# Performance work log

Hardware: AMD Instinct MI355X
Metric: run time of the kernel (lower is better)

Reference implementation:

```python
import jax, jax.numpy as jnp
import numpy as np

B, T, D, H, HORIZON, OUT = 1024, 64, 128, 128, 24, 1
ATT = 64  # attention MLP hidden size


def _p(key, shape, scale=0.05):
    return scale * jax.random.normal(key, shape, dtype=jnp.float32)


def setup_inputs() -> dict:
    ks = jax.random.split(jax.random.key(0), 20)
    return dict(
        X=jax.random.normal(ks[0], (B, T, D), jnp.float32),
        y_hist=jax.random.normal(ks[1], (B, T), jnp.float32),
        We_w=_p(ks[2], (ATT, 2 * H + 1)), We_b=_p(ks[3], (ATT,)),
        ve_w=_p(ks[4], (1, ATT)), ve_b=_p(ks[5], (1,)),
        enc_Wih=_p(ks[6], (4 * H, D)), enc_Whh=_p(ks[7], (4 * H, H)),
        enc_bih=_p(ks[8], (4 * H,)), enc_bhh=_p(ks[9], (4 * H,)),
        dec_Wih=_p(ks[10], (4 * H, 1)), dec_Whh=_p(ks[11], (4 * H, H)),
        dec_bih=_p(ks[12], (4 * H,)), dec_bhh=_p(ks[13], (4 * H,)),
        Wd_w=_p(ks[14], (ATT, 3 * H)), Wd_b=_p(ks[15], (ATT,)),
        vd_w=_p(ks[16], (1, ATT)), vd_b=_p(ks[17], (1,)),
        fc_w=_p(ks[18], (OUT, 2 * H + T)), fc_b=_p(ks[19], (OUT,)),
    )


def _lstm_cell(x, h, c, Wih, Whh, bih, bhh):
    # torch.nn.LSTMCell gate order: i, f, g, o
    gates = x @ Wih.T + bih + h @ Whh.T + bhh
    i, f, g, o = jnp.split(gates, 4, axis=1)
    c2 = jax.nn.sigmoid(f) * c + jax.nn.sigmoid(i) * jnp.tanh(g)
    h2 = jax.nn.sigmoid(o) * jnp.tanh(c2)
    return h2, c2


def _forward(X, y_hist, We_w, We_b, ve_w, ve_b,
             enc_Wih, enc_Whh, enc_bih, enc_bhh,
             dec_Wih, dec_Whh, dec_bih, dec_bhh,
             Wd_w, Wd_b, vd_w, vd_b, fc_w, fc_b):
    batch = X.shape[0]
    # --- encoder with input attention (vectorized over the per-k python loop) ---
    W_hs = We_w[:, :2 * H]       # weights on [h_prev, s_prev]
    w_feat = We_w[:, 2 * H]      # weight on the scalar feature, shape (ATT,)

    def enc_step(carry, x_t):
        h, c = carry
        base = jnp.concatenate([h, c], axis=1) @ W_hs.T + We_b        # (B, ATT)
        energy = jnp.tanh(base[:, None, :] + x_t[:, :, None] * w_feat)  # (B, D, ATT)
        scores = energy @ ve_w[0] + ve_b[0]                            # (B, D)
        alpha = jax.nn.softmax(scores, axis=1)
        x_tilde = alpha * x_t
        h2, c2 = _lstm_cell(x_tilde, h, c, enc_Wih, enc_Whh, enc_bih, enc_bhh)
        return (h2, c2), h2

    h0 = jnp.zeros((batch, H), X.dtype)
    c0 = jnp.zeros((batch, H), X.dtype)
    _, enc_h = jax.lax.scan(enc_step, (h0, c0), X.transpose(1, 0, 2))
    enc_hiddens = enc_h.transpose(1, 0, 2)  # (B, T, H)

    # --- decoder with temporal attention ---
    # Wd_w columns ordered as cat([encoder_hiddens, d_prev, c_prev])
    enc_proj = jnp.einsum('bth,kh->btk', enc_hiddens, Wd_w[:, :H])  # (B, T, ATT)
    Wd_d, Wd_c = Wd_w[:, H:2 * H], Wd_w[:, 2 * H:]

    def dec_step(carry, _):
        d, cc, y_prev = carry
        dc = d @ Wd_d.T + cc @ Wd_c.T + Wd_b                # (B, ATT)
        energy = jnp.tanh(enc_proj + dc[:, None, :])         # (B, T, ATT)
        score = energy @ vd_w[0] + vd_b[0]                   # (B, T)
        beta = jax.nn.softmax(score, axis=1)
        context = jnp.einsum('bt,bth->bh', beta, enc_hiddens)  # (B, H)
        d2, cc2 = _lstm_cell(y_prev, d, cc, dec_Wih, dec_Whh, dec_bih, dec_bhh)
        fc_in = jnp.concatenate([d2, context, y_hist], axis=1)  # (B, 2H+T)
        out = fc_in @ fc_w.T + fc_b                              # (B, 1)
        return (d2, cc2, out), out

    d0 = jnp.zeros((batch, H), X.dtype)
    cd0 = jnp.zeros((batch, H), X.dtype)
    y0 = y_hist[:, -1:]
    _, outs = jax.lax.scan(dec_step, (d0, cd0, y0), None, length=HORIZON)
    return outs.transpose(1, 0, 2)  # (B, horizon, output_dim)


def reference(X, y_hist, We_w, We_b, ve_w, ve_b,
              enc_Wih, enc_Whh, enc_bih, enc_bhh,
              dec_Wih, dec_Whh, dec_bih, dec_bhh,
              Wd_w, Wd_b, vd_w, vd_b, fc_w, fc_b):
    return _forward(X, y_hist, We_w, We_b, ve_w, ve_b,
                    enc_Wih, enc_Whh, enc_bih, enc_bhh,
                    dec_Wih, dec_Whh, dec_bih, dec_bhh,
                    Wd_w, Wd_b, vd_w, vd_b, fc_w, fc_b)
```

## Files before the change

### kernel.cpp

```cpp
#include <hip/hip_runtime.h>
#include <hip/hip_bf16.h>


#define B_    1024
#define T_    64
#define D_    128
#define H_    128
#define HOR_  24
#define ATT_  64
#define BB    4
#define LOG2E 1.4426950408889634f
#define C127  (1.f/127.f)
#define KLAG  8.245856315e-05f

typedef float f32x4  __attribute__((ext_vector_type(4)));
typedef short bf16x8 __attribute__((ext_vector_type(8)));
typedef int   i32x4  __attribute__((ext_vector_type(4)));

#define MFMA16(a,b,c) __builtin_amdgcn_mfma_f32_16x16x32_bf16((a),(b),(c),0,0,0)
#define MFMAI8(a,b,c) __builtin_amdgcn_mfma_i32_16x16x64_i8((a),(b),(c),0,0,0)

#define WHS_E    0
#define WDDC_E   16384
#define WDENC_E  32768
#define WENC8_B  81920
#define WDEC8_B  212992
#define SENC_B   278528
#define SDEC_B   280576

__device__ __forceinline__ short f2b(float f) {
  union { float f; unsigned u; } c; c.f = f;
  unsigned r = c.u + 0x7fffu + ((c.u >> 16) & 1u);
  return (short)(r >> 16);
}
__device__ __forceinline__ float b2f(short s) {
  union { unsigned u; float f; } c; c.u = ((unsigned)(unsigned short)s) << 16;
  return c.f;
}
__device__ __forceinline__ float fexp2(float x) { return __builtin_amdgcn_exp2f(x); }
__device__ __forceinline__ float frcp (float x) { return __builtin_amdgcn_rcpf(x); }
__device__ __forceinline__ float tanh_acc(float x) {
  float e = fexp2(x * 2.885390081777927f);
  return 1.f - 2.f * frcp(1.f + e);
}
__device__ __forceinline__ float sigm(float x) {
  return frcp(1.f + fexp2(-LOG2E * x));
}

template<int CTRL>
__device__ __forceinline__ float dppmov(float v) {
  return __builtin_bit_cast(float,
      __builtin_amdgcn_mov_dpp(__builtin_bit_cast(int, v), CTRL, 0xF, 0xF, true));
}
__device__ __forceinline__ float swz16(float v) {
  return __builtin_bit_cast(float,
      __builtin_amdgcn_ds_swizzle(__builtin_bit_cast(int, v), 0x401F));
}
__device__ __forceinline__ float wsum64(float v) {
  v += dppmov<0xB1>(v);
  v += dppmov<0x4E>(v);
  v += dppmov<0x141>(v);
  v += dppmov<0x140>(v);
  v += swz16(v);
  v += __shfl_xor(v, 32, 64);
  return v;
}
__device__ __forceinline__ float wmax64(float v) {
  v = fmaxf(v, dppmov<0xB1>(v));
  v = fmaxf(v, dppmov<0x4E>(v));
  v = fmaxf(v, dppmov<0x141>(v));
  v = fmaxf(v, dppmov<0x140>(v));
  v = fmaxf(v, swz16(v));
  v = fmaxf(v, __shfl_xor(v, 32, 64));
  return v;
}
__device__ __forceinline__ float gsum8(float v) {
  v += dppmov<0xB1>(v);
  v += dppmov<0x4E>(v);
  v += dppmov<0x141>(v);
  return v;
}

__global__ void prep_bf(const float* __restrict__ We_w,
                        const float* __restrict__ Wd_w,
                        char* __restrict__ ws8) {
  int e = blockIdx.x * 256 + threadIdx.x;
  if (e >= 40960) return;
  short* f16 = (short*)ws8;
  int region = e >> 14;
  int er = e & 16383;
  int fi = er >> 9, li = (er >> 3) & 63, jq = er & 7;
  int kt = fi >> 2, nt = fi & 3;
  int k = kt * 32 + ((li >> 4) << 3) + jq, n = nt * 16 + (li & 15);
  float v;
  if (region == 0)      v = We_w[n * 257 + k];
  else if (region == 1) v = (k < 128) ? Wd_w[n * 384 + 128 + k]
                                      : Wd_w[n * 384 + 256 + (k - 128)];
  else                  v = Wd_w[n * 384 + k];
  f16[e] = f2b(v);
}

__global__ void prep_q(const float* __restrict__ enc_Wih,
                       const float* __restrict__ enc_Whh,
                       const float* __restrict__ dec_Whh,
                       char* __restrict__ ws8) {
  int gw = (blockIdx.x * 256 + threadIdx.x) >> 6;
  int lane = threadIdx.x & 63;
  if (gw < 512) {
    int n = gw;
    float v[4]; float m = 0.f;
#pragma unroll
    for (int q = 0; q < 4; ++q) {
      int k = lane * 4 + q;
      v[q] = (k < 128) ? enc_Wih[n * 128 + k] : enc_Whh[n * 128 + (k - 128)];
      m = fmaxf(m, fabsf(v[q]));
    }
    m = wmax64(m);
    if (lane == 0) ((float*)(ws8 + SENC_B))[n] = m * C127;
    float inv = m > 0.f ? 127.f / m : 0.f;
    char* dst = ws8 + WENC8_B;
#pragma unroll
    for (int q = 0; q < 4; ++q) {
      int k = lane * 4 + q;
      int kt = k >> 6, grp = (k >> 4) & 3, b = k & 15, l16 = (n & 15) | (grp << 4);
      dst[((kt * 32 + (n >> 4)) * 64 + l16) * 16 + b] = (char)(int)rintf(v[q] * inv);
    }
  } else if (gw < 1024) {
    int n = gw - 512;
    float v[2]; float m = 0.f;
#pragma unroll
    for (int q = 0; q < 2; ++q) {
      int k = lane * 2 + q;
      v[q] = dec_Whh[n * 128 + k];
      m = fmaxf(m, fabsf(v[q]));
    }
    m = wmax64(m);
    if (lane == 0) ((float*)(ws8 + SDEC_B))[n] = m * C127;
    float inv = m > 0.f ? 127.f / m : 0.f;
    char* dst = ws8 + WDEC8_B;
#pragma unroll
    for (int q = 0; q < 2; ++q) {
      int k = lane * 2 + q;
      int kt = k >> 6, grp = (k >> 4) & 3, b = k & 15, l16 = (n & 15) | (grp << 4);
      dst[((kt * 32 + (n >> 4)) * 64 + l16) * 16 + b] = (char)(int)rintf(v[q] * inv);
    }
  }
}

__global__ __launch_bounds__(512, 2)
void da_rnn(const float* __restrict__ X, const float* __restrict__ y_hist,
            const float* __restrict__ We_w, const float* __restrict__ We_b,
            const float* __restrict__ ve_w,
            const float* __restrict__ enc_bih, const float* __restrict__ enc_bhh,
            const float* __restrict__ dec_Wih,
            const float* __restrict__ dec_bih, const float* __restrict__ dec_bhh,
            const float* __restrict__ Wd_b, const float* __restrict__ vd_w,
            const float* __restrict__ fc_w, const float* __restrict__ fc_b,
            const char* __restrict__ ws8, float* __restrict__ out) {
  const short* f16  = (const short*)ws8;
  const i32x4* enc8 = (const i32x4*)(ws8 + WENC8_B);
  const i32x4* dec8 = (const i32x4*)(ws8 + WDEC8_B);
  const float* senc = (const float*)(ws8 + SENC_B);
  const float* sdec = (const float*)(ws8 + SDEC_B);

  __shared__ __align__(16) char  s_A8[16][272];
  __shared__ __align__(16) short s_Ahc[16][264];
  __shared__ short s_projT[4][64][65];
  __shared__ short s_encht[4][128][66];
  __shared__ __align__(16) float s_gates[4][528];
  __shared__ __align__(16) float s_base[4][72];
  __shared__ float s_beta[4][64];
  __shared__ float s_xr[4];
  __shared__ float2 s_wv[64];
  __shared__ __align__(16) float s_web[64];
  __shared__ float s_vd[64];
  __shared__ __align__(16) float s_wdb[64];
  __shared__ float s_se[512], s_sd[512];
  __shared__ float s_encb[512], s_decb[512], s_dwih[512];
  __shared__ float s_fcw[320];

  const int tid  = threadIdx.x;
  const int lane = tid & 63;
  const int w    = tid >> 6;
  const int b0   = blockIdx.x * BB;

  if (tid < 64) {
    s_wv[tid]  = make_float2(We_w[tid * 257 + 256], ve_w[tid]);
    s_web[tid] = We_b[tid];
    s_vd[tid]  = vd_w[tid];
    s_wdb[tid] = Wd_b[tid];
  }
  if (tid < 320) s_fcw[tid] = fc_w[tid];
  s_se[tid]   = senc[tid];
  s_sd[tid]   = sdec[tid];
  s_encb[tid] = enc_bih[tid] + enc_bhh[tid];
  s_decb[tid] = dec_bih[tid] + dec_bhh[tid];
  s_dwih[tid] = dec_Wih[tid];
  for (int i = tid; i < (16 * 272) / 4; i += 512) ((int*)s_A8)[i] = 0;
  for (int i = tid; i < (16 * 264) / 2; i += 512) ((int*)s_Ahc)[i] = 0;
  if (tid < 256) s_base[tid >> 6][tid & 63] = We_b[tid & 63];

  i32x4 wg[4][4];
#pragma unroll
  for (int kt = 0; kt < 4; ++kt)
#pragma unroll
    for (int i = 0; i < 4; ++i)
      wg[kt][i] = enc8[(kt * 32 + (w + 8 * i)) * 64 + lane];
  bf16x8 wb[8], wp[4];
  if (w < 4) {
#pragma unroll
    for (int kt = 0; kt < 8; ++kt)
      wb[kt] = *(const bf16x8*)(f16 + WHS_E + ((kt * 4 + w) * 64 + lane) * 8);
  } else {
#pragma unroll
    for (int kt = 0; kt < 4; ++kt)
      wp[kt] = *(const bf16x8*)(f16 + WDENC_E + ((kt * 4 + (w - 4)) * 64 + lane) * 8);
  }

  float h0 = 0.f, c0 = 0.f, h1 = 0.f, c1 = 0.f;
  float xf0 = 0.f, xf1 = 0.f, xi = 0.f;
  const float* Xr = X + (size_t)(b0 + (w & 3)) * T_ * D_;
  if (w < 4) {
    xf0 = Xr[lane]; xf1 = Xr[64 + lane];
    xi = 6.f * cosf((2 * (lane >> 3) + 1) * 0.19634954084936207f);
  }
  i32x4 ahp[4];
#pragma unroll
  for (int i = 0; i < 4; ++i) ahp[i] = (i32x4){0, 0, 0, 0};
  __syncthreads();

  float se_p[8], eb_p[8];
  f32x4 webq = {0.f, 0.f, 0.f, 0.f};
  if (w < 4) {
#pragma unroll
    for (int j = 0; j < 8; ++j) {
      se_p[j] = s_se[lane + 64 * j];
      eb_p[j] = s_encb[lane + 64 * j];
    }
    webq = *(const f32x4*)&s_web[(w << 4) + ((lane >> 4) << 2)];
  }

  for (int t = 0; t < T_; ++t) {
    float x0, x1;
    if (w < 4) {
      x0 = xf0; x1 = xf1;
      const int kc = lane & 7;
      float p = 0.f;
      const float4* wvp = (const float4*)&s_wv[kc * 8];
      const float4* bp  = (const float4*)&s_base[w][kc * 8];
      float4 bA = bp[0], bB = bp[1];
#pragma unroll
      for (int q = 0; q < 4; ++q) {
        float4 wv = wvp[q];
        float bb0 = (q < 2) ? ((q & 1) ? bA.z : bA.x) : ((q & 1) ? bB.z : bB.x);
        float bb1 = (q < 2) ? ((q & 1) ? bA.w : bA.y) : ((q & 1) ? bB.w : bB.y);
        p += wv.y * tanh_acc(fmaf(xi, wv.x, bb0));
        p += wv.w * tanh_acc(fmaf(xi, wv.z, bb1));
      }
      p = gsum8(p);
      float f0 = __shfl(p,  0, 64), f1 = __shfl(p,  8, 64);
      float f2 = __shfl(p, 16, 64), f3 = __shfl(p, 24, 64);
      float f4 = __shfl(p, 32, 64), f5 = __shfl(p, 40, 64);
      float f6 = __shfl(p, 48, 64), f7 = __shfl(p, 56, 64);
      float e0, e1;
      {
        const float xb[8] = { 5.884711682f, 4.988817674f, 3.333421398f, 1.170541932f,
                             -1.170541932f, -3.333421398f, -4.988817674f, -5.884711682f};
        const float wbar[8] = { 0.1950903220f, -0.5555702330f, 0.8314696123f, -0.9807852804f,
                                0.9807852804f, -0.8314696123f, 0.5555702330f, -0.1950903220f};
        float fw[8] = {f0 * wbar[0], f1 * wbar[1], f2 * wbar[2], f3 * wbar[3],
                       f4 * wbar[4], f5 * wbar[5], f6 * wbar[6], f7 * wbar[7]};
        float u0 = fminf(fmaxf(x0, -6.f), 6.f), u1 = fminf(fmaxf(x1, -6.f), 6.f);
        float d0[8], d1[8], P0[8], P1[8];
        float pre0 = 1.f, pre1 = 1.f;
#pragma unroll
        for (int i = 0; i < 8; ++i) {
          d0[i] = u0 - xb[i]; d1[i] = u1 - xb[i];
          P0[i] = pre0;       P1[i] = pre1;
          pre0 *= d0[i];      pre1 *= d1[i];
        }
        float suf0 = 1.f, suf1 = 1.f, acc0 = 0.f, acc1 = 0.f;
#pragma unroll
        for (int i = 7; i >= 0; --i) {
          acc0 = fmaf(fw[i] * P0[i], suf0, acc0);
          acc1 = fmaf(fw[i] * P1[i], suf1, acc1);
          suf0 *= d0[i];
          suf1 *= d1[i];
        }
        e0 = fexp2(acc0 * KLAG);
        e1 = fexp2(acc1 * KLAG);
      }
      float sum = wsum64(e0 + e1);
      float mx  = wmax64(fmaxf(e0 * fabsf(x0), e1 * fabsf(x1)));
      float inv = mx > 0.f ? 127.f * frcp(mx) : 0.f;
      s_A8[w][lane]      = (char)(int)rintf(x0 * e0 * inv);
      s_A8[w][64 + lane] = (char)(int)rintf(x1 * e1 * inv);
      if (lane == 0) s_xr[w] = mx * frcp(127.f * sum);
    }
    __syncthreads();
    {
      i32x4 a0 = *(const i32x4*)&s_A8[lane & 15][  0 + ((lane >> 4) << 4)];
      i32x4 a1 = *(const i32x4*)&s_A8[lane & 15][ 64 + ((lane >> 4) << 4)];
      i32x4 ax[4];
#pragma unroll
      for (int i = 0; i < 4; ++i) {
        i32x4 z = {0, 0, 0, 0};
        ax[i] = MFMAI8(wg[1][i], a1, MFMAI8(wg[0][i], a0, z));
      }
      float sx = s_xr[lane & 3];
      if ((lane & 15) < 4) {
        int cb = (lane >> 4) << 2;
#pragma unroll
        for (int i = 0; i < 4; ++i) {
          f32x4 v;
#pragma unroll
          for (int r = 0; r < 4; ++r)
            v[r] = fmaf(sx, (float)ax[i][r], C127 * (float)ahp[i][r]);
          *(f32x4*)&s_gates[lane & 15][(w + 8 * i) * 16 + cb] = v;
        }
      }
    }
    __syncthreads();
    if (w < 4) {
      float gi0 = fmaf(s_gates[w][lane]      , se_p[0], eb_p[0]);
      float gi1 = fmaf(s_gates[w][lane + 64] , se_p[1], eb_p[1]);
      float gf0 = fmaf(s_gates[w][lane + 128], se_p[2], eb_p[2]);
      float gf1 = fmaf(s_gates[w][lane + 192], se_p[3], eb_p[3]);
      float gg0 = fmaf(s_gates[w][lane + 256], se_p[4], eb_p[4]);
      float gg1 = fmaf(s_gates[w][lane + 320], se_p[5], eb_p[5]);
      float go0 = fmaf(s_gates[w][lane + 384], se_p[6], eb_p[6]);
      float go1 = fmaf(s_gates[w][lane + 448], se_p[7], eb_p[7]);
      c0 = sigm(gf0) * c0 + sigm(gi0) * tanh_acc(gg0);
      h0 = sigm(go0) * tanh_acc(c0);
      c1 = sigm(gf1) * c1 + sigm(gi1) * tanh_acc(gg1);
      h1 = sigm(go1) * tanh_acc(c1);
      s_Ahc[w][lane]        = f2b(h0);
      s_Ahc[w][lane + 64]   = f2b(h1);
      s_Ahc[w][lane + 128]  = f2b(c0);
      s_Ahc[w][lane + 192]  = f2b(c1);
      s_A8[w][128 + lane]      = (char)(int)rintf(h0 * 127.f);
      s_A8[w][128 + lane + 64] = (char)(int)rintf(h1 * 127.f);
      s_encht[w][lane][t]      = f2b(h0);
      s_encht[w][lane + 64][t] = f2b(h1);
    }
    __syncthreads();
    {
      i32x4 pa2 = *(const i32x4*)&s_A8[lane & 15][128 + ((lane >> 4) << 4)];
      i32x4 pa3 = *(const i32x4*)&s_A8[lane & 15][192 + ((lane >> 4) << 4)];
#pragma unroll
      for (int i = 0; i < 4; ++i) {
        i32x4 z = {0, 0, 0, 0};
        ahp[i] = MFMAI8(wg[3][i], pa3, MFMAI8(wg[2][i], pa2, z));
      }
    }
    if (w < 4) {
      if (t < T_ - 1) {
        xf0 = Xr[(t + 1) * D_ + lane];
        xf1 = Xr[(t + 1) * D_ + 64 + lane];
      }
      f32x4 acc = {0.f, 0.f, 0.f, 0.f}, acc2 = {0.f, 0.f, 0.f, 0.f};
#pragma unroll
      for (int kt = 0; kt < 4; ++kt) {
        bf16x8 a = *(const bf16x8*)&s_Ahc[lane & 15][kt * 32 + ((lane >> 4) << 3)];
        acc = MFMA16(wb[kt], a, acc);
      }
#pragma unroll
      for (int kt = 4; kt < 8; ++kt) {
        bf16x8 a = *(const bf16x8*)&s_Ahc[lane & 15][kt * 32 + ((lane >> 4) << 3)];
        acc2 = MFMA16(wb[kt], a, acc2);
      }
      if ((lane & 15) < 4) {
        f32x4 v = acc + acc2 + webq;
        *(f32x4*)&s_base[lane & 15][(w << 4) + ((lane >> 4) << 2)] = v;
      }
    } else {
      f32x4 acc = {0.f, 0.f, 0.f, 0.f};
#pragma unroll
      for (int kt = 0; kt < 4; ++kt) {
        bf16x8 a = *(const bf16x8*)&s_Ahc[lane & 15][kt * 32 + ((lane >> 4) << 3)];
        acc = MFMA16(a, wp[kt], acc);
      }
      if (lane < 16) {
        int katt = (w - 4) * 16 + lane;
#pragma unroll
        for (int r = 0; r < 4; ++r) s_projT[r][katt][t] = f2b(acc[r]);
      }
    }
    __syncthreads();
  }

  {
    int r = tid >> 7, j = tid & 127;
    s_Ahc[r][j] = 0; s_Ahc[r][128 + j] = 0; s_A8[r][j] = 0;
  }
  i32x4 wdg[2][8];
  bf16x8 wdc[8];
  float yp = 0.f, yhd = 0.f;
  float sdC_p[8];
  f32x4 wdbq = {0.f, 0.f, 0.f, 0.f};
  if (w >= 4) {
#pragma unroll
    for (int kt = 0; kt < 2; ++kt)
#pragma unroll
      for (int i = 0; i < 8; ++i)
        wdg[kt][i] = dec8[(kt * 32 + ((w - 4) * 8 + i)) * 64 + lane];
  } else {
#pragma unroll
    for (int kt = 0; kt < 8; ++kt)
      wdc[kt] = *(const bf16x8*)(f16 + WDDC_E + ((kt * 4 + w) * 64 + lane) * 8);
#pragma unroll
    for (int j = 0; j < 8; ++j) sdC_p[j] = s_sd[lane + 64 * j] * C127;
    wdbq = *(const f32x4*)&s_wdb[(w << 4) + ((lane >> 4) << 2)];
    yp = y_hist[(b0 + w) * T_ + (T_ - 1)];
    float pp = s_fcw[256 + lane] * y_hist[(b0 + w) * T_ + lane];
    yhd = wsum64(pp) + fc_b[0];
  }
  float dd0 = 0.f, dc0 = 0.f, dd1 = 0.f, dc1 = 0.f;
  __syncthreads();

  for (int hs = 0; hs < HOR_; ++hs) {
    if (w >= 4) {
      i32x4 a0 = *(const i32x4*)&s_A8[lane & 15][ 0 + ((lane >> 4) << 4)];
      i32x4 a1 = *(const i32x4*)&s_A8[lane & 15][64 + ((lane >> 4) << 4)];
#pragma unroll
      for (int i = 0; i < 8; ++i) {
        i32x4 z = {0, 0, 0, 0};
        i32x4 ac = MFMAI8(wdg[1][i], a1, MFMAI8(wdg[0][i], a0, z));
        if ((lane & 15) < 4) {
          f32x4 v = {(float)ac[0], (float)ac[1], (float)ac[2], (float)ac[3]};
          *(f32x4*)&s_gates[lane & 15][(((w - 4) * 8 + i) << 4) + ((lane >> 4) << 2)] = v;
        }
      }
    } else {
      f32x4 acc = {0.f, 0.f, 0.f, 0.f}, acc2 = {0.f, 0.f, 0.f, 0.f};
#pragma unroll
      for (int kt = 0; kt < 4; ++kt) {
        bf16x8 a = *(const bf16x8*)&s_Ahc[lane & 15][kt * 32 + ((lane >> 4) << 3)];
        acc = MFMA16(wdc[kt], a, acc);
      }
#pragma unroll
      for (int kt = 4; kt < 8; ++kt) {
        bf16x8 a = *(const bf16x8*)&s_Ahc[lane & 15][kt * 32 + ((lane >> 4) << 3)];
        acc2 = MFMA16(wdc[kt], a, acc2);
      }
      if ((lane & 15) < 4) {
        f32x4 v = acc + acc2 + wdbq;
        *(f32x4*)&s_base[lane & 15][(w << 4) + ((lane >> 4) << 2)] = v;
      }
    }
    __syncthreads();
    if (w < 4) {
      float sA = 0.f, sB = 0.f, sC = 0.f, sD = 0.f;
#pragma unroll 4
      for (int k = 0; k < 64; k += 4) {
        sA += s_vd[k]     * tanh_acc(b2f(s_projT[w][k][lane])     + s_base[w][k]);
        sB += s_vd[k + 1] * tanh_acc(b2f(s_projT[w][k + 1][lane]) + s_base[w][k + 1]);
        sC += s_vd[k + 2] * tanh_acc(b2f(s_projT[w][k + 2][lane]) + s_base[w][k + 2]);
        sD += s_vd[k + 3] * tanh_acc(b2f(s_projT[w][k + 3][lane]) + s_base[w][k + 3]);
      }
      float s = (sA + sB) + (sC + sD);
      float e = fexp2(s * LOG2E);
      float ssum = wsum64(e);
      s_beta[w][lane] = e * frcp(ssum);
      float cx0a = 0.f, cx0b = 0.f, cx1a = 0.f, cx1b = 0.f;
      const short* e0p = &s_encht[w][lane][0];
      const short* e1p = &s_encht[w][lane + 64][0];
#pragma unroll 8
      for (int tp = 0; tp < 32; ++tp) {
        float2 bta = *(const float2*)&s_beta[w][2 * tp];
        short2 h0v = *(const short2*)&e0p[2 * tp];
        short2 h1v = *(const short2*)&e1p[2 * tp];
        cx0a = fmaf(bta.x, b2f(h0v.x), cx0a); cx0b = fmaf(bta.y, b2f(h0v.y), cx0b);
        cx1a = fmaf(bta.x, b2f(h1v.x), cx1a); cx1b = fmaf(bta.y, b2f(h1v.y), cx1b);
      }
      float cx0 = cx0a + cx0b, cx1 = cx1a + cx1b;
      float gi0 = s_gates[w][lane]       * sdC_p[0] + s_decb[lane]       + yp * s_dwih[lane];
      float gi1 = s_gates[w][lane + 64]  * sdC_p[1] + s_decb[lane + 64]  + yp * s_dwih[lane + 64];
      float gf0 = s_gates[w][lane + 128] * sdC_p[2] + s_decb[lane + 128] + yp * s_dwih[lane + 128];
      float gf1 = s_gates[w][lane + 192] * sdC_p[3] + s_decb[lane + 192] + yp * s_dwih[lane + 192];
      float gg0 = s_gates[w][lane + 256] * sdC_p[4] + s_decb[lane + 256] + yp * s_dwih[lane + 256];
      float gg1 = s_gates[w][lane + 320] * sdC_p[5] + s_decb[lane + 320] + yp * s_dwih[lane + 320];
      float go0 = s_gates[w][lane + 384] * sdC_p[6] + s_decb[lane + 384] + yp * s_dwih[lane + 384];
      float go1 = s_gates[w][lane + 448] * sdC_p[7] + s_decb[lane + 448] + yp * s_dwih[lane + 448];
      dc0 = sigm(gf0) * dc0 + sigm(gi0) * tanh_acc(gg0);
      dd0 = sigm(go0) * tanh_acc(dc0);
      dc1 = sigm(gf1) * dc1 + sigm(gi1) * tanh_acc(gg1);
      dd1 = sigm(go1) * tanh_acc(dc1);
      float pf = s_fcw[lane] * dd0 + s_fcw[64 + lane] * dd1
               + s_fcw[128 + lane] * cx0 + s_fcw[192 + lane] * cx1;
      pf = wsum64(pf);
      float o = pf + yhd;
      if (lane == 0) out[(b0 + w) * HOR_ + hs] = o;
      yp = o;
      s_Ahc[w][lane]       = f2b(dd0);
      s_Ahc[w][lane + 64]  = f2b(dd1);
      s_Ahc[w][lane + 128] = f2b(dc0);
      s_Ahc[w][lane + 192] = f2b(dc1);
      s_A8[w][lane]      = (char)(int)rintf(dd0 * 127.f);
      s_A8[w][lane + 64] = (char)(int)rintf(dd1 * 127.f);
    }
    __syncthreads();
  }
}

extern "C" void kernel_launch(void* const* d_in, const int* in_sizes, int n_in,
                              void* d_out, int out_size, void* d_ws, size_t ws_size,
                              hipStream_t stream) {
  (void)in_sizes; (void)n_in; (void)out_size; (void)ws_size;
  const float* X       = (const float*)d_in[0];
  const float* y_hist  = (const float*)d_in[1];
  const float* We_w    = (const float*)d_in[2];
  const float* We_b    = (const float*)d_in[3];
  const float* ve_w    = (const float*)d_in[4];
  const float* enc_Wih = (const float*)d_in[6];
  const float* enc_Whh = (const float*)d_in[7];
  const float* enc_bih = (const float*)d_in[8];
  const float* enc_bhh = (const float*)d_in[9];
  const float* dec_Wih = (const float*)d_in[10];
  const float* dec_Whh = (const float*)d_in[11];
  const float* dec_bih = (const float*)d_in[12];
  const float* dec_bhh = (const float*)d_in[13];
  const float* Wd_w    = (const float*)d_in[14];
  const float* Wd_b    = (const float*)d_in[15];
  const float* vd_w    = (const float*)d_in[16];
  const float* fc_w    = (const float*)d_in[18];
  const float* fc_b    = (const float*)d_in[19];

  char* ws8  = (char*)d_ws;
  float* out = (float*)d_out;

  prep_bf<<<160, 256, 0, stream>>>(We_w, Wd_w, ws8);
  prep_q <<<256, 256, 0, stream>>>(enc_Wih, enc_Whh, dec_Whh, ws8);
  da_rnn <<<B_ / BB, 512, 0, stream>>>(X, y_hist, We_w, We_b, ve_w,
                                       enc_bih, enc_bhh, dec_Wih, dec_bih, dec_bhh,
                                       Wd_b, vd_w, fc_w, fc_b, ws8, out);
}
```

Before: 314.4 us.

## Spread LSTM cell and decoder attention across all eight waves, defer output

The encoder LSTM cell update now runs on all 8 waves, each lane handling one hidden unit instead of two, so the four otherwise idle waves share the elementwise gate work. In the decoder, the attention score and softmax move to waves 4-7 and run in the phase after the gate MFMAs. The context reduction and FC output for step hs are deferred into step hs+1's first phase, with a final epilogue writing the last output. Decoder bias and Wih values are cached in registers. This shortens the serial critical path per timestep at the cost of more register pressure and a restructured dependency chain across phases.

Measured after the change: 300.2 us. -4.5%, faster.

```diff
diff --git a/kernel.cpp b/kernel.cpp
--- a/kernel.cpp
+++ b/kernel.cpp
@@ -217,28 +217,28 @@
       wp[kt] = *(const bf16x8*)(f16 + WDENC_E + ((kt * 4 + (w - 4)) * 64 + lane) * 8);
   }
 
-  float h0 = 0.f, c0 = 0.f, h1 = 0.f, c1 = 0.f;
   float xf0 = 0.f, xf1 = 0.f, xi = 0.f;
   const float* Xr = X + (size_t)(b0 + (w & 3)) * T_ * D_;
   if (w < 4) {
     xf0 = Xr[lane]; xf1 = Xr[64 + lane];
     xi = 6.f * cosf((2 * (lane >> 3) + 1) * 0.19634954084936207f);
   }
+  float cstE = 0.f;
+  const int rE = w & 3;
+  const int fE = ((w >> 2) << 6) + lane;
   i32x4 ahp[4];
 #pragma unroll
   for (int i = 0; i < 4; ++i) ahp[i] = (i32x4){0, 0, 0, 0};
   __syncthreads();
 
-  float se_p[8], eb_p[8];
+  float seE[4], ebE[4];
+#pragma unroll
+  for (int g = 0; g < 4; ++g) {
+    seE[g] = s_se[fE + 128 * g];
+    ebE[g] = s_encb[fE + 128 * g];
+  }
   f32x4 webq = {0.f, 0.f, 0.f, 0.f};
-  if (w < 4) {
-#pragma unroll
-    for (int j = 0; j < 8; ++j) {
-      se_p[j] = s_se[lane + 64 * j];
-      eb_p[j] = s_encb[lane + 64 * j];
-    }
-    webq = *(const f32x4*)&s_web[(w << 4) + ((lane >> 4) << 2)];
-  }
+  if (w < 4) webq = *(const f32x4*)&s_web[(w << 4) + ((lane >> 4) << 2)];
 
   for (int t = 0; t < T_; ++t) {
     float x0, x1;
@@ -321,27 +321,17 @@
       }
     }
     __syncthreads();
-    if (w < 4) {
-      float gi0 = fmaf(s_gates[w][lane]      , se_p[0], eb_p[0]);
-      float gi1 = fmaf(s_gates[w][lane + 64] , se_p[1], eb_p[1]);
-      float gf0 = fmaf(s_gates[w][lane + 128], se_p[2], eb_p[2]);
-      float gf1 = fmaf(s_gates[w][lane + 192], se_p[3], eb_p[3]);
-      float gg0 = fmaf(s_gates[w][lane + 256], se_p[4], eb_p[4]);
-      float gg1 = fmaf(s_gates[w][lane + 320], se_p[5], eb_p[5]);
-      float go0 = fmaf(s_gates[w][lane + 384], se_p[6], eb_p[6]);
-      float go1 = fmaf(s_gates[w][lane + 448], se_p[7], eb_p[7]);
-      c0 = sigm(gf0) * c0 + sigm(gi0) * tanh_acc(gg0);
-      h0 = sigm(go0) * tanh_acc(c0);
-      c1 = sigm(gf1) * c1 + sigm(gi1) * tanh_acc(gg1);
-      h1 = sigm(go1) * tanh_acc(c1);
-      s_Ahc[w][lane]        = f2b(h0);
-      s_Ahc[w][lane + 64]   = f2b(h1);
-      s_Ahc[w][lane + 128]  = f2b(c0);
-      s_Ahc[w][lane + 192]  = f2b(c1);
-      s_A8[w][128 + lane]      = (char)(int)rintf(h0 * 127.f);
-      s_A8[w][128 + lane + 64] = (char)(int)rintf(h1 * 127.f);
-      s_encht[w][lane][t]      = f2b(h0);
-      s_encht[w][lane + 64][t] = f2b(h1);
+    {
+      float g_i = fmaf(s_gates[rE][fE]      , seE[0], ebE[0]);
+      float g_f = fmaf(s_gates[rE][fE + 128], seE[1], ebE[1]);
+      float g_g = fmaf(s_gates[rE][fE + 256], seE[2], ebE[2]);
+      float g_o = fmaf(s_gates[rE][fE + 384], seE[3], ebE[3]);
+      cstE = sigm(g_f) * cstE + sigm(g_i) * tanh_acc(g_g);
+      float h = sigm(g_o) * tanh_acc(cstE);
+      s_Ahc[rE][fE]        = f2b(h);
+      s_Ahc[rE][128 + fE]  = f2b(cstE);
+      s_A8[rE][128 + fE]   = (char)(int)rintf(h * 127.f);
+      s_encht[rE][fE][t]   = f2b(h);
     }
     __syncthreads();
     {
@@ -396,7 +386,7 @@
   i32x4 wdg[2][8];
   bf16x8 wdc[8];
   float yp = 0.f, yhd = 0.f;
-  float sdC_p[8];
+  float sdC_p[8], db_p[8], dw_p[8];
   f32x4 wdbq = {0.f, 0.f, 0.f, 0.f};
   if (w >= 4) {
 #pragma unroll
@@ -409,7 +399,11 @@
     for (int kt = 0; kt < 8; ++kt)
       wdc[kt] = *(const bf16x8*)(f16 + WDDC_E + ((kt * 4 + w) * 64 + lane) * 8);
 #pragma unroll
-    for (int j = 0; j < 8; ++j) sdC_p[j] = s_sd[lane + 64 * j] * C127;
+    for (int j = 0; j < 8; ++j) {
+      sdC_p[j] = s_sd[lane + 64 * j] * C127;
+      db_p[j]  = s_decb[lane + 64 * j];
+      dw_p[j]  = s_dwih[lane + 64 * j];
+    }
     wdbq = *(const f32x4*)&s_wdb[(w << 4) + ((lane >> 4) << 2)];
     yp = y_hist[(b0 + w) * T_ + (T_ - 1)];
     float pp = s_fcw[256 + lane] * y_hist[(b0 + w) * T_ + lane];
@@ -432,6 +426,26 @@
         }
       }
     } else {
+      if (hs > 0) {
+        float cx0a = 0.f, cx0b = 0.f, cx1a = 0.f, cx1b = 0.f;
+        const short* e0p = &s_encht[w][lane][0];
+        const short* e1p = &s_encht[w][lane + 64][0];
+#pragma unroll 8
+        for (int tp = 0; tp < 32; ++tp) {
+          float2 bta = *(const float2*)&s_beta[w][2 * tp];
+          short2 h0v = *(const short2*)&e0p[2 * tp];
+          short2 h1v = *(const short2*)&e1p[2 * tp];
+          cx0a = fmaf(bta.x, b2f(h0v.x), cx0a); cx0b = fmaf(bta.y, b2f(h0v.y), cx0b);
+          cx1a = fmaf(bta.x, b2f(h1v.x), cx1a); cx1b = fmaf(bta.y, b2f(h1v.y), cx1b);
+        }
+        float cx0 = cx0a + cx0b, cx1 = cx1a + cx1b;
+        float pf = s_fcw[lane] * dd0 + s_fcw[64 + lane] * dd1
+                 + s_fcw[128 + lane] * cx0 + s_fcw[192 + lane] * cx1;
+        pf = wsum64(pf);
+        float o = pf + yhd;
+        if (lane == 0) out[(b0 + w) * HOR_ + (hs - 1)] = o;
+        yp = o;
+      }
       f32x4 acc = {0.f, 0.f, 0.f, 0.f}, acc2 = {0.f, 0.f, 0.f, 0.f};
 #pragma unroll
       for (int kt = 0; kt < 4; ++kt) {
@@ -450,56 +464,59 @@
     }
     __syncthreads();
     if (w < 4) {
-      float sA = 0.f, sB = 0.f, sC = 0.f, sD = 0.f;
-#pragma unroll 4
-      for (int k = 0; k < 64; k += 4) {
-        sA += s_vd[k]     * tanh_acc(b2f(s_projT[w][k][lane])     + s_base[w][k]);
-        sB += s_vd[k + 1] * tanh_acc(b2f(s_projT[w][k + 1][lane]) + s_base[w][k + 1]);
-        sC += s_vd[k + 2] * tanh_acc(b2f(s_projT[w][k + 2][lane]) + s_base[w][k + 2]);
-        sD += s_vd[k + 3] * tanh_acc(b2f(s_projT[w][k + 3][lane]) + s_base[w][k + 3]);
-      }
-      float s = (sA + sB) + (sC + sD);
-      float e = fexp2(s * LOG2E);
-      float ssum = wsum64(e);
-      s_beta[w][lane] = e * frcp(ssum);
-      float cx0a = 0.f, cx0b = 0.f, cx1a = 0.f, cx1b = 0.f;
-      const short* e0p = &s_encht[w][lane][0];
-      const short* e1p = &s_encht[w][lane + 64][0];
-#pragma unroll 8
-      for (int tp = 0; tp < 32; ++tp) {
-        float2 bta = *(const float2*)&s_beta[w][2 * tp];
-        short2 h0v = *(const short2*)&e0p[2 * tp];
-        short2 h1v = *(const short2*)&e1p[2 * tp];
-        cx0a = fmaf(bta.x, b2f(h0v.x), cx0a); cx0b = fmaf(bta.y, b2f(h0v.y), cx0b);
-        cx1a = fmaf(bta.x, b2f(h1v.x), cx1a); cx1b = fmaf(bta.y, b2f(h1v.y), cx1b);
-      }
-      float cx0 = cx0a + cx0b, cx1 = cx1a + cx1b;
-      float gi0 = s_gates[w][lane]       * sdC_p[0] + s_decb[lane]       + yp * s_dwih[lane];
-      float gi1 = s_gates[w][lane + 64]  * sdC_p[1] + s_decb[lane + 64]  + yp * s_dwih[lane + 64];
-      float gf0 = s_gates[w][lane + 128] * sdC_p[2] + s_decb[lane + 128] + yp * s_dwih[lane + 128];
-      float gf1 = s_gates[w][lane + 192] * sdC_p[3] + s_decb[lane + 192] + yp * s_dwih[lane + 192];
-      float gg0 = s_gates[w][lane + 256] * sdC_p[4] + s_decb[lane + 256] + yp * s_dwih[lane + 256];
-      float gg1 = s_gates[w][lane + 320] * sdC_p[5] + s_decb[lane + 320] + yp * s_dwih[lane + 320];
-      float go0 = s_gates[w][lane + 384] * sdC_p[6] + s_decb[lane + 384] + yp * s_dwih[lane + 384];
-      float go1 = s_gates[w][lane + 448] * sdC_p[7] + s_decb[lane + 448] + yp * s_dwih[lane + 448];
+      float gi0 = s_gates[w][lane]       * sdC_p[0] + db_p[0] + yp * dw_p[0];
+      float gi1 = s_gates[w][lane + 64]  * sdC_p[1] + db_p[1] + yp * dw_p[1];
+      float gf0 = s_gates[w][lane + 128] * sdC_p[2] + db_p[2] + yp * dw_p[2];
+      float gf1 = s_gates[w][lane + 192] * sdC_p[3] + db_p[3] + yp * dw_p[3];
+      float gg0 = s_gates[w][lane + 256] * sdC_p[4] + db_p[4] + yp * dw_p[4];
+      float gg1 = s_gates[w][lane + 320] * sdC_p[5] + db_p[5] + yp * dw_p[5];
+      float go0 = s_gates[w][lane + 384] * sdC_p[6] + db_p[6] + yp * dw_p[6];
+      float go1 = s_gates[w][lane + 448] * sdC_p[7] + db_p[7] + yp * dw_p[7];
       dc0 = sigm(gf0) * dc0 + sigm(gi0) * tanh_acc(gg0);
       dd0 = sigm(go0) * tanh_acc(dc0);
       dc1 = sigm(gf1) * dc1 + sigm(gi1) * tanh_acc(gg1);
       dd1 = sigm(go1) * tanh_acc(dc1);
-      float pf = s_fcw[lane] * dd0 + s_fcw[64 + lane] * dd1
-               + s_fcw[128 + lane] * cx0 + s_fcw[192 + lane] * cx1;
-      pf = wsum64(pf);
-      float o = pf + yhd;
-      if (lane == 0) out[(b0 + w) * HOR_ + hs] = o;
-      yp = o;
       s_Ahc[w][lane]       = f2b(dd0);
       s_Ahc[w][lane + 64]  = f2b(dd1);
       s_Ahc[w][lane + 128] = f2b(dc0);
       s_Ahc[w][lane + 192] = f2b(dc1);
       s_A8[w][lane]      = (char)(int)rintf(dd0 * 127.f);
       s_A8[w][lane + 64] = (char)(int)rintf(dd1 * 127.f);
+    } else {
+      const int r = w - 4;
+      float sA = 0.f, sB = 0.f, sC = 0.f, sD = 0.f;
+#pragma unroll 4
+      for (int k = 0; k < 64; k += 4) {
+        sA += s_vd[k]     * tanh_acc(b2f(s_projT[r][k][lane])     + s_base[r][k]);
+        sB += s_vd[k + 1] * tanh_acc(b2f(s_projT[r][k + 1][lane]) + s_base[r][k + 1]);
+        sC += s_vd[k + 2] * tanh_acc(b2f(s_projT[r][k + 2][lane]) + s_base[r][k + 2]);
+        sD += s_vd[k + 3] * tanh_acc(b2f(s_projT[r][k + 3][lane]) + s_base[r][k + 3]);
+      }
+      float s = (sA + sB) + (sC + sD);
+      float e = fexp2(s * LOG2E);
+      float ssum = wsum64(e);
+      s_beta[r][lane] = e * frcp(ssum);
     }
     __syncthreads();
+  }
+  if (w < 4) {
+    float cx0a = 0.f, cx0b = 0.f, cx1a = 0.f, cx1b = 0.f;
+    const short* e0p = &s_encht[w][lane][0];
+    const short* e1p = &s_encht[w][lane + 64][0];
+#pragma unroll 8
+    for (int tp = 0; tp < 32; ++tp) {
+      float2 bta = *(const float2*)&s_beta[w][2 * tp];
+      short2 h0v = *(const short2*)&e0p[2 * tp];
+      short2 h1v = *(const short2*)&e1p[2 * tp];
+      cx0a = fmaf(bta.x, b2f(h0v.x), cx0a); cx0b = fmaf(bta.y, b2f(h0v.y), cx0b);
+      cx1a = fmaf(bta.x, b2f(h1v.x), cx1a); cx1b = fmaf(bta.y, b2f(h1v.y), cx1b);
+    }
+    float cx0 = cx0a + cx0b, cx1 = cx1a + cx1b;
+    float pf = s_fcw[lane] * dd0 + s_fcw[64 + lane] * dd1
+             + s_fcw[128 + lane] * cx0 + s_fcw[192 + lane] * cx1;
+    pf = wsum64(pf);
+    float o = pf + yhd;
+    if (lane == 0) out[(b0 + w) * HOR_ + (HOR_ - 1)] = o;
   }
 }
 
```
